# Optimization experiments

Hardware: AMD Instinct MI355X
Metric: run time of the kernel (lower is better)

The kernel has to match this reference:

```python
import jax, jax.numpy as jnp
import numpy as np

HEAD_SIZE = 64
N_EMBED = 768
B, T = 16, 2048


def setup_inputs() -> dict:
    key = jax.random.key(0)
    ks = jax.random.split(key, 7)
    return {
        "x": jax.random.normal(ks[0], (B, T, N_EMBED), dtype=jnp.float32),
        "v1": jax.random.normal(ks[1], (B, T, HEAD_SIZE), dtype=jnp.float32),
        "Wk": jax.random.normal(ks[2], (N_EMBED, HEAD_SIZE), dtype=jnp.float32) * 0.02,
        "Wq": jax.random.normal(ks[3], (N_EMBED, HEAD_SIZE), dtype=jnp.float32) * 0.02,
        "Wv": jax.random.normal(ks[4], (N_EMBED, HEAD_SIZE), dtype=jnp.float32) * 0.02,
        "Wproj": jax.random.normal(ks[5], (HEAD_SIZE, HEAD_SIZE), dtype=jnp.float32) * 0.02,
        "bproj": jnp.zeros((HEAD_SIZE,), dtype=jnp.float32),
        "lamb": jnp.float32(0.5),
    }


def reference(x, v1, Wk, Wq, Wv, Wproj, bproj, lamb):
    # x: [B, T, C]; single-head causal attention with value-residual mixing.
    k = x @ Wk  # [B, T, H]
    q = x @ Wq
    v = x @ Wv
    v = (1.0 - lamb) * v + lamb * v1  # value-residual mix
    scale = jnp.float32(1.0 / np.sqrt(HEAD_SIZE))
    w = jnp.einsum("bth,bsh->bts", q, k) * scale  # [B, T, T]
    t = x.shape[1]
    causal = jnp.tril(jnp.ones((t, t), dtype=bool))  # [T, T]
    w = jnp.where(causal, w, jnp.float32(-jnp.inf))
    w = jax.nn.softmax(w, axis=-1)
    # dropout is identity in eval mode
    out = jnp.einsum("bts,bsh->bth", w, v)  # [B, T, H]
    return out @ Wproj + bproj, v1
```

## Files before the change

### kernel.cpp

```cpp
#include <hip/hip_runtime.h>
#include <hip/hip_bf16.h>


constexpr int BATCH = 16;
constexpr int TSEQ  = 2048;
constexpr int CEMB  = 768;
constexpr int HS    = 64;
constexpr size_t NTOK    = (size_t)BATCH * TSEQ;
constexpr size_t OUTHALF = NTOK * HS;

typedef __bf16 bf16x4 __attribute__((ext_vector_type(4)));
typedef __bf16 bf16x8 __attribute__((ext_vector_type(8)));
typedef float  f32x4  __attribute__((ext_vector_type(4)));
typedef float  f32x16 __attribute__((ext_vector_type(16)));
typedef int    i32x4  __attribute__((ext_vector_type(4)));

__global__ __launch_bounds__(256) void prep_kernel(
    const float* __restrict__ wk, const float* __restrict__ wq,
    const float* __restrict__ wv, const float* __restrict__ wproj,
    __bf16* __restrict__ wt, __bf16* __restrict__ wpt)
{
    __shared__ __bf16 t[64][66];
    const int bid = blockIdx.x;
    if (bid < 36) {
        const int m = bid / 12, c0 = (bid % 12) * 64;
        const float* src = (m == 0) ? wk : (m == 1) ? wq : wv;
        for (int i = threadIdx.x; i < 4096; i += 256) {
            const int c = i >> 6, h = i & 63;
            t[c][h] = (__bf16)src[(size_t)(c0 + c) * HS + h];
        }
        __syncthreads();
        for (int i = threadIdx.x; i < 4096; i += 256) {
            const int h = i >> 6, c = i & 63;
            wt[(size_t)m * HS * CEMB + (size_t)h * CEMB + c0 + c] = t[c][h];
        }
    } else {
        for (int i = threadIdx.x; i < 4096; i += 256) {
            const int h = i >> 6, hp = i & 63;
            t[h][hp] = (__bf16)wproj[i];
        }
        __syncthreads();
        for (int i = threadIdx.x; i < 4096; i += 256) {
            const int hp = i >> 6, h = i & 63;
            wpt[i] = t[h][hp];
        }
    }
}

__global__ __launch_bounds__(256, 2) void qkv_kernel(
    const float* __restrict__ x,
    const float* __restrict__ v1,
    const __bf16* __restrict__ wt,
    const float* __restrict__ lamb_p,
    __bf16* __restrict__ kk,
    __bf16* __restrict__ qq,
    __bf16* __restrict__ vt)
{
    __shared__ __bf16 xl[2][64][88];

    const int wave = threadIdx.x >> 6;
    const int lane = threadIdx.x & 63;
    const int l16  = lane & 15;
    const int quad = lane >> 4;
    const size_t row0 = (size_t)blockIdx.x * 64;

    const int tok_s = threadIdx.x >> 2;
    const int cq    = threadIdx.x & 3;
    const float* xsrc = x + (row0 + tok_s) * CEMB + cq * 16;

    const __bf16* wbase[3];
    #pragma unroll
    for (int m = 0; m < 3; ++m)
        wbase[m] = wt + ((size_t)m * HS + wave * 16 + l16) * CEMB + quad * 8;

    f32x4 acc[3][4];
    #pragma unroll
    for (int m = 0; m < 3; ++m)
        #pragma unroll
        for (int rt = 0; rt < 4; ++rt)
            acc[m][rt] = (f32x4){0.f, 0.f, 0.f, 0.f};

    {
        f32x4 t0 = *(const f32x4*)(xsrc);
        f32x4 t1 = *(const f32x4*)(xsrc + 4);
        f32x4 t2 = *(const f32x4*)(xsrc + 8);
        f32x4 t3 = *(const f32x4*)(xsrc + 12);
        bf16x8 lo, hi;
        #pragma unroll
        for (int i = 0; i < 4; ++i) {
            lo[i] = (__bf16)t0[i]; lo[i + 4] = (__bf16)t1[i];
            hi[i] = (__bf16)t2[i]; hi[i + 4] = (__bf16)t3[i];
        }
        *(bf16x8*)&xl[0][tok_s][cq * 16]     = lo;
        *(bf16x8*)&xl[0][tok_s][cq * 16 + 8] = hi;
    }
    bf16x8 wc[3][2];
    #pragma unroll
    for (int m = 0; m < 3; ++m)
        #pragma unroll
        for (int ks = 0; ks < 2; ++ks)
            wc[m][ks] = *(const bf16x8*)(wbase[m] + ks * 32);
    __syncthreads();

    for (int c0 = 0; c0 < CEMB; c0 += 64) {
        const int buf = (c0 >> 6) & 1;
        const bool notlast = (c0 + 64 < CEMB);

        f32x4 nx0, nx1, nx2, nx3;
        bf16x8 wn[3][2];
        if (notlast) {
            const float* xs = xsrc + c0 + 64;
            nx0 = *(const f32x4*)(xs);
            nx1 = *(const f32x4*)(xs + 4);
            nx2 = *(const f32x4*)(xs + 8);
            nx3 = *(const f32x4*)(xs + 12);
            #pragma unroll
            for (int m = 0; m < 3; ++m)
                #pragma unroll
                for (int ks = 0; ks < 2; ++ks)
                    wn[m][ks] = *(const bf16x8*)(wbase[m] + c0 + 64 + ks * 32);
        }

        #pragma unroll
        for (int ks = 0; ks < 2; ++ks) {
            bf16x8 a[4];
            #pragma unroll
            for (int rt = 0; rt < 4; ++rt)
                a[rt] = *(const bf16x8*)&xl[buf][rt * 16 + l16][ks * 32 + quad * 8];
            #pragma unroll
            for (int m = 0; m < 3; ++m)
                #pragma unroll
                for (int rt = 0; rt < 4; ++rt)
                    acc[m][rt] = __builtin_amdgcn_mfma_f32_16x16x32_bf16(
                        a[rt], wc[m][ks], acc[m][rt], 0, 0, 0);
        }

        if (notlast) {
            bf16x8 lo, hi;
            #pragma unroll
            for (int i = 0; i < 4; ++i) {
                lo[i] = (__bf16)nx0[i]; lo[i + 4] = (__bf16)nx1[i];
                hi[i] = (__bf16)nx2[i]; hi[i + 4] = (__bf16)nx3[i];
            }
            *(bf16x8*)&xl[buf ^ 1][tok_s][cq * 16]     = lo;
            *(bf16x8*)&xl[buf ^ 1][tok_s][cq * 16 + 8] = hi;
            #pragma unroll
            for (int m = 0; m < 3; ++m)
                #pragma unroll
                for (int ks = 0; ks < 2; ++ks)
                    wc[m][ks] = wn[m][ks];
            __syncthreads();
        }
    }

    const float lam = lamb_p[0];
    const int col = wave * 16 + l16;
    const int b  = (int)(row0 >> 11);
    __bf16* vtb = vt + (size_t)b * HS * TSEQ + (size_t)col * TSEQ;
    #pragma unroll
    for (int rt = 0; rt < 4; ++rt) {
        const size_t tok0 = row0 + rt * 16 + quad * 4;
        bf16x4 pk;
        #pragma unroll
        for (int r = 0; r < 4; ++r) {
            const size_t idx = (tok0 + r) * HS + col;
            kk[idx] = (__bf16)acc[0][rt][r];
            qq[idx] = (__bf16)acc[1][rt][r];
            pk[r] = (__bf16)((1.0f - lam) * acc[2][rt][r] + lam * v1[idx]);
        }
        *(bf16x4*)(vtb + (tok0 & 2047)) = pk;
    }
}

__device__ __forceinline__ int pk2(float lo, float hi) {
    unsigned short a = __builtin_bit_cast(unsigned short, (__bf16)lo);
    unsigned short b = __builtin_bit_cast(unsigned short, (__bf16)hi);
    return (int)((((unsigned)b) << 16) | (unsigned)a);
}
__device__ __forceinline__ bf16x8 make_bfrag(const float* p, int hi) {
    const int a0 = pk2(p[0], p[1]), a1 = pk2(p[2], p[3]);
    const int b0 = pk2(p[4], p[5]), b1 = pk2(p[6], p[7]);
    const int pa0 = __shfl_xor(a0, 32), pa1 = __shfl_xor(a1, 32);
    const int pb0 = __shfl_xor(b0, 32), pb1 = __shfl_xor(b1, 32);
    i32x4 w;
    w[0] = hi ? pb0 : a0;
    w[1] = hi ? pb1 : a1;
    w[2] = hi ? b0  : pa0;
    w[3] = hi ? b1  : pa1;
    return __builtin_bit_cast(bf16x8, w);
}

__global__ __launch_bounds__(256, 2) void attn_kernel(
    const __bf16* __restrict__ q,
    const __bf16* __restrict__ k,
    const __bf16* __restrict__ vt,
    const __bf16* __restrict__ wpt,
    const float* __restrict__ bproj,
    float* __restrict__ y)
{
    __shared__ float olds[4][64][32];
    __shared__ float mred[4][32];
    __shared__ float lred[4][32];

    const int b    = blockIdx.x >> 5;
    const int jp   = blockIdx.x & 31;
    const int wave = threadIdx.x >> 6;
    const int lane = threadIdx.x & 63;
    const int l31  = lane & 31;
    const int hi   = lane >> 5;
    const int hi8  = hi * 8;

    const __bf16* kb = k  + (size_t)b * TSEQ * HS;
    const __bf16* vb = vt + (size_t)b * HS * TSEQ;
    const float sc2 = 0.125f * 1.44269504f;

    bf16x8 wf[4];
    if (wave < 2) {
        const __bf16* wp = wpt + (size_t)(wave * 32 + l31) * HS + hi8;
        #pragma unroll
        for (int c = 0; c < 4; ++c) wf[c] = *(const bf16x8*)(wp + c * 16);
    }

    for (int pass = 0; pass < 2; ++pass) {
        const int j = pass ? (63 - jp) : jp;
        const size_t tok0 = (size_t)b * TSEQ + (size_t)j * 32;

        const __bf16* qp = q + (tok0 + l31) * HS + hi8;
        bf16x8 qf[4];
        #pragma unroll
        for (int c = 0; c < 4; ++c) qf[c] = *(const bf16x8*)(qp + c * 16);

        f32x16 o0, o1;
        #pragma unroll
        for (int r = 0; r < 16; ++r) { o0[r] = 0.f; o1[r] = 0.f; }
        float m_i = -1e30f, l_i = 0.f;

        bf16x8 kf[4], kn[4];
        if (wave <= j) {
            const __bf16* kp = kb + (size_t)(wave * 32 + l31) * HS + hi8;
            #pragma unroll
            for (int c = 0; c < 4; ++c) kf[c] = *(const bf16x8*)(kp + c * 16);
        }

        for (int t = wave; t <= j; t += 4) {
            const int s0 = t * 32;
            bf16x8 vf[4];
            #pragma unroll
            for (int ht = 0; ht < 2; ++ht)
                #pragma unroll
                for (int c2 = 0; c2 < 2; ++c2)
                    vf[ht * 2 + c2] = *(const bf16x8*)(vb
                        + (size_t)(ht * 32 + l31) * TSEQ + s0 + c2 * 16 + hi8);
            if (t + 4 <= j) {
                const __bf16* kp = kb + (size_t)((t + 4) * 32 + l31) * HS + hi8;
                #pragma unroll
                for (int c = 0; c < 4; ++c) kn[c] = *(const bf16x8*)(kp + c * 16);
            }

            f32x16 s;
            #pragma unroll
            for (int r = 0; r < 16; ++r) s[r] = 0.f;
            #pragma unroll
            for (int c = 0; c < 4; ++c)
                s = __builtin_amdgcn_mfma_f32_32x32x16_bf16(kf[c], qf[c], s, 0, 0, 0);

            float p[16];
            if (t == j) {
                #pragma unroll
                for (int r = 0; r < 16; ++r) {
                    const int krow = (r & 3) + 8 * (r >> 2) + 4 * hi;
                    p[r] = (krow <= l31) ? s[r] * sc2 : -1e30f;
                }
            } else {
                #pragma unroll
                for (int r = 0; r < 16; ++r) p[r] = s[r] * sc2;
            }

            float x0 = fmaxf(p[0], p[1]),   x1 = fmaxf(p[2], p[3]);
            float x2 = fmaxf(p[4], p[5]),   x3 = fmaxf(p[6], p[7]);
            float x4 = fmaxf(p[8], p[9]),   x5 = fmaxf(p[10], p[11]);
            float x6 = fmaxf(p[12], p[13]), x7 = fmaxf(p[14], p[15]);
            float mx = fmaxf(fmaxf(fmaxf(x0, x1), fmaxf(x2, x3)),
                             fmaxf(fmaxf(x4, x5), fmaxf(x6, x7)));
            mx = fmaxf(mx, __shfl_xor(mx, 32));

            if (!__all(mx <= m_i + 8.f)) {
                const float mn = fmaxf(m_i, mx);
                const float alpha = exp2f(m_i - mn);
                m_i = mn;
                l_i *= alpha;
                #pragma unroll
                for (int r = 0; r < 16; ++r) { o0[r] *= alpha; o1[r] *= alpha; }
            }

            #pragma unroll
            for (int r = 0; r < 16; ++r) p[r] = exp2f(p[r] - m_i);

            float r0 = (p[0] + p[1]) + (p[2] + p[3]);
            float r1 = (p[4] + p[5]) + (p[6] + p[7]);
            float r2 = (p[8] + p[9]) + (p[10] + p[11]);
            float r3 = (p[12] + p[13]) + (p[14] + p[15]);
            float rs = (r0 + r1) + (r2 + r3);
            rs += __shfl_xor(rs, 32);
            l_i += rs;

            const bf16x8 fb0 = make_bfrag(&p[0], hi);
            const bf16x8 fb1 = make_bfrag(&p[8], hi);

            o0 = __builtin_amdgcn_mfma_f32_32x32x16_bf16(vf[0], fb0, o0, 0, 0, 0);
            o0 = __builtin_amdgcn_mfma_f32_32x32x16_bf16(vf[1], fb1, o0, 0, 0, 0);
            o1 = __builtin_amdgcn_mfma_f32_32x32x16_bf16(vf[2], fb0, o1, 0, 0, 0);
            o1 = __builtin_amdgcn_mfma_f32_32x32x16_bf16(vf[3], fb1, o1, 0, 0, 0);

            if (t + 4 <= j) {
                #pragma unroll
                for (int c = 0; c < 4; ++c) kf[c] = kn[c];
            }
        }

        #pragma unroll
        for (int r = 0; r < 16; ++r) {
            const int row = (r & 3) + 8 * (r >> 2) + 4 * hi;
            olds[wave][row][l31]      = o0[r];
            olds[wave][row + 32][l31] = o1[r];
        }
        if (lane < 32) { mred[wave][lane] = m_i; lred[wave][lane] = l_i; }
        __syncthreads();

        if (wave < 2) {
            float mw[4], lw[4];
            #pragma unroll
            for (int w = 0; w < 4; ++w) { mw[w] = mred[w][l31]; lw[w] = lred[w][l31]; }
            const float mg = fmaxf(fmaxf(mw[0], mw[1]), fmaxf(mw[2], mw[3]));
            float g[4], lg = 0.f;
            #pragma unroll
            for (int w = 0; w < 4; ++w) { g[w] = exp2f(mw[w] - mg); lg += g[w] * lw[w]; }
            const float inv = 1.0f / lg;

            float on[32];
            #pragma unroll
            for (int r = 0; r < 16; ++r) {
                const int row = (r & 3) + 8 * (r >> 2) + 4 * hi;
                float a0 = 0.f, a1 = 0.f;
                #pragma unroll
                for (int w = 0; w < 4; ++w) {
                    a0 += g[w] * olds[w][row][l31];
                    a1 += g[w] * olds[w][row + 32][l31];
                }
                on[r]      = a0 * inv;
                on[r + 16] = a1 * inv;
            }

            f32x16 res;
            #pragma unroll
            for (int r = 0; r < 16; ++r) res[r] = 0.f;
            #pragma unroll
            for (int c = 0; c < 4; ++c) {
                const bf16x8 ob = make_bfrag(&on[c * 8], hi);
                res = __builtin_amdgcn_mfma_f32_32x32x16_bf16(wf[c], ob, res, 0, 0, 0);
            }

            float* yp = y + (tok0 + l31) * HS + wave * 32;
            #pragma unroll
            for (int grp = 0; grp < 4; ++grp) {
                const f32x4 bb = *(const f32x4*)(bproj + wave * 32 + grp * 8 + 4 * hi);
                f32x4 o4;
                #pragma unroll
                for (int rr = 0; rr < 4; ++rr) o4[rr] = res[grp * 4 + rr] + bb[rr];
                *(f32x4*)(yp + grp * 8 + 4 * hi) = o4;
            }
        }
        __syncthreads();
    }
}

__global__ __launch_bounds__(256) void copy_kernel(
    const float* __restrict__ src, float* __restrict__ dst)
{
    const size_t i = ((size_t)blockIdx.x * 256 + threadIdx.x) * 4;
    *(f32x4*)(dst + i) = *(const f32x4*)(src + i);
}

extern "C" void kernel_launch(void* const* d_in, const int* in_sizes, int n_in,
                              void* d_out, int out_size, void* d_ws, size_t ws_size,
                              hipStream_t stream) {
    const float* x     = (const float*)d_in[0];
    const float* v1    = (const float*)d_in[1];
    const float* wk    = (const float*)d_in[2];
    const float* wq    = (const float*)d_in[3];
    const float* wv    = (const float*)d_in[4];
    const float* wproj = (const float*)d_in[5];
    const float* bproj = (const float*)d_in[6];
    const float* lamb  = (const float*)d_in[7];

    float* out = (float*)d_out;
    __bf16* kp  = (__bf16*)(out + OUTHALF);
    __bf16* vtp = kp + OUTHALF;
    __bf16* qp  = (__bf16*)d_ws;
    __bf16* wt  = qp + OUTHALF;
    __bf16* wpt = wt + (size_t)3 * HS * CEMB;

    prep_kernel<<<dim3(37), dim3(256), 0, stream>>>(wk, wq, wv, wproj, wt, wpt);

    qkv_kernel<<<dim3((int)(NTOK / 64)), dim3(256), 0, stream>>>(
        x, v1, wt, lamb, kp, qp, vtp);

    attn_kernel<<<dim3(BATCH * 32), dim3(256), 0, stream>>>(
        qp, kp, vtp, wpt, bproj, out);

    copy_kernel<<<dim3((int)(OUTHALF / (256 * 4))), dim3(256), 0, stream>>>(
        v1, out + OUTHALF);
}
```

Before: 229.7 us.

## Fuse v1 passthrough copy into QKV kernel and prefetch V tiles with MFMA priority

```diff
diff --git a/kernel.cpp b/kernel.cpp
--- a/kernel.cpp
+++ b/kernel.cpp
@@ -54,7 +54,8 @@
     const float* __restrict__ lamb_p,
     __bf16* __restrict__ kk,
     __bf16* __restrict__ qq,
-    __bf16* __restrict__ vt)
+    __bf16* __restrict__ vt,
+    float* __restrict__ v1out)
 {
     __shared__ __bf16 xl[2][64][88];
 
@@ -164,9 +165,11 @@
         #pragma unroll
         for (int r = 0; r < 4; ++r) {
             const size_t idx = (tok0 + r) * HS + col;
+            const float v1v = v1[idx];
             kk[idx] = (__bf16)acc[0][rt][r];
             qq[idx] = (__bf16)acc[1][rt][r];
-            pk[r] = (__bf16)((1.0f - lam) * acc[2][rt][r] + lam * v1[idx]);
+            pk[r] = (__bf16)((1.0f - lam) * acc[2][rt][r] + lam * v1v);
+            if (v1out) v1out[idx] = v1v;
         }
         *(bf16x4*)(vtb + (tok0 & 2047)) = pk;
     }
@@ -235,34 +238,44 @@
         for (int r = 0; r < 16; ++r) { o0[r] = 0.f; o1[r] = 0.f; }
         float m_i = -1e30f, l_i = 0.f;
 
-        bf16x8 kf[4], kn[4];
+        bf16x8 kf[4], kn[4], vf[4], vn[4];
         if (wave <= j) {
-            const __bf16* kp = kb + (size_t)(wave * 32 + l31) * HS + hi8;
+            const int s0 = wave * 32;
+            const __bf16* kp = kb + (size_t)(s0 + l31) * HS + hi8;
             #pragma unroll
             for (int c = 0; c < 4; ++c) kf[c] = *(const bf16x8*)(kp + c * 16);
-        }
-
-        for (int t = wave; t <= j; t += 4) {
-            const int s0 = t * 32;
-            bf16x8 vf[4];
             #pragma unroll
             for (int ht = 0; ht < 2; ++ht)
                 #pragma unroll
                 for (int c2 = 0; c2 < 2; ++c2)
                     vf[ht * 2 + c2] = *(const bf16x8*)(vb
                         + (size_t)(ht * 32 + l31) * TSEQ + s0 + c2 * 16 + hi8);
-            if (t + 4 <= j) {
-                const __bf16* kp = kb + (size_t)((t + 4) * 32 + l31) * HS + hi8;
+        }
+
+        for (int t = wave; t <= j; t += 4) {
+            const int s0 = t * 32;
+            const bool more = (t + 4 <= j);
+            if (more) {
+                const int sn = s0 + 128;
+                const __bf16* kp = kb + (size_t)(sn + l31) * HS + hi8;
                 #pragma unroll
                 for (int c = 0; c < 4; ++c) kn[c] = *(const bf16x8*)(kp + c * 16);
+                #pragma unroll
+                for (int ht = 0; ht < 2; ++ht)
+                    #pragma unroll
+                    for (int c2 = 0; c2 < 2; ++c2)
+                        vn[ht * 2 + c2] = *(const bf16x8*)(vb
+                            + (size_t)(ht * 32 + l31) * TSEQ + sn + c2 * 16 + hi8);
             }
 
             f32x16 s;
             #pragma unroll
             for (int r = 0; r < 16; ++r) s[r] = 0.f;
+            __builtin_amdgcn_s_setprio(1);
             #pragma unroll
             for (int c = 0; c < 4; ++c)
                 s = __builtin_amdgcn_mfma_f32_32x32x16_bf16(kf[c], qf[c], s, 0, 0, 0);
+            __builtin_amdgcn_s_setprio(0);
 
             float p[16];
             if (t == j) {
@@ -307,14 +320,16 @@
             const bf16x8 fb0 = make_bfrag(&p[0], hi);
             const bf16x8 fb1 = make_bfrag(&p[8], hi);
 
+            __builtin_amdgcn_s_setprio(1);
             o0 = __builtin_amdgcn_mfma_f32_32x32x16_bf16(vf[0], fb0, o0, 0, 0, 0);
             o0 = __builtin_amdgcn_mfma_f32_32x32x16_bf16(vf[1], fb1, o0, 0, 0, 0);
             o1 = __builtin_amdgcn_mfma_f32_32x32x16_bf16(vf[2], fb0, o1, 0, 0, 0);
             o1 = __builtin_amdgcn_mfma_f32_32x32x16_bf16(vf[3], fb1, o1, 0, 0, 0);
-
-            if (t + 4 <= j) {
-                #pragma unroll
-                for (int c = 0; c < 4; ++c) kf[c] = kn[c];
+            __builtin_amdgcn_s_setprio(0);
+
+            if (more) {
+                #pragma unroll
+                for (int c = 0; c < 4; ++c) { kf[c] = kn[c]; vf[c] = vn[c]; }
             }
         }
 
@@ -394,20 +409,37 @@
     const float* lamb  = (const float*)d_in[7];
 
     float* out = (float*)d_out;
-    __bf16* kp  = (__bf16*)(out + OUTHALF);
-    __bf16* vtp = kp + OUTHALF;
+
     __bf16* qp  = (__bf16*)d_ws;
     __bf16* wt  = qp + OUTHALF;
     __bf16* wpt = wt + (size_t)3 * HS * CEMB;
+    const size_t base_elems = OUTHALF + (size_t)3 * HS * CEMB + (size_t)HS * HS;
+    const size_t need_bytes = (base_elems + 2 * OUTHALF) * sizeof(__bf16);
+
+    __bf16* kp;
+    __bf16* vtp;
+    float*  v1out;
+    const bool fused_v1 = (ws_size >= need_bytes);
+    if (fused_v1) {
+        kp    = wpt + (size_t)HS * HS;
+        vtp   = kp + OUTHALF;
+        v1out = out + OUTHALF;
+    } else {
+        kp    = (__bf16*)(out + OUTHALF);
+        vtp   = kp + OUTHALF;
+        v1out = nullptr;
+    }
 
     prep_kernel<<<dim3(37), dim3(256), 0, stream>>>(wk, wq, wv, wproj, wt, wpt);
 
     qkv_kernel<<<dim3((int)(NTOK / 64)), dim3(256), 0, stream>>>(
-        x, v1, wt, lamb, kp, qp, vtp);
+        x, v1, wt, lamb, kp, qp, vtp, v1out);
 
     attn_kernel<<<dim3(BATCH * 32), dim3(256), 0, stream>>>(
         qp, kp, vtp, wpt, bproj, out);
 
-    copy_kernel<<<dim3((int)(OUTHALF / (256 * 4))), dim3(256), 0, stream>>>(
-        v1, out + OUTHALF);
-}
+    if (!fused_v1) {
+        copy_kernel<<<dim3((int)(OUTHALF / (256 * 4))), dim3(256), 0, stream>>>(
+            v1, out + OUTHALF);
+    }
+}
```

Result: slower. 237.5 us (+3.4%).
